# Kernel optimization log

Hardware: AMD Instinct MI355X
Metric: run time of the kernel (lower is better)

## Reference

```python
import jax, jax.numpy as jnp
import numpy as np

N = 100_000          # number of nodes
E = 3_200_000        # number of edges (avg degree 32)
IN_CH = 128
OUT_CH = 128


def setup_inputs() -> dict:
    key = jax.random.key(0)
    k1, k2, k3, k4 = jax.random.split(key, 4)
    x = jax.random.normal(k1, (N, IN_CH), dtype=jnp.float32)
    edge_index = jax.random.randint(k2, (2, E), 0, N, dtype=jnp.int32)
    # torch nn.Linear weights have shape [out_features, in_features]
    W_theta = jax.random.normal(k3, (OUT_CH, IN_CH), dtype=jnp.float32) / np.sqrt(IN_CH).astype(np.float32)
    W_phi = jax.random.normal(k4, (OUT_CH, OUT_CH), dtype=jnp.float32) / np.sqrt(OUT_CH).astype(np.float32)
    return {"x": x, "edge_index": edge_index, "W_theta": W_theta, "W_phi": W_phi}


def reference(x, edge_index, W_theta, W_phi):
    row, col = edge_index[0], edge_index[1]
    rel_pos = x[row] - x[col]                       # [E, in]
    rel_t = rel_pos @ W_theta.T                     # [E, out]
    aggr = jax.ops.segment_max(rel_t, row, num_segments=N)  # [N, out], -inf for empty segments
    # torch_scatter.scatter_max leaves empty segments at 0
    aggr = jnp.where(jnp.isneginf(aggr), jnp.zeros((), dtype=aggr.dtype), aggr)
    return aggr @ W_phi.T                           # [N, out]
```

## Files before the change

kernel.cpp:

```cpp
#include <hip/hip_runtime.h>
#include <stdint.h>

#define N_NODES 100000
#define N_EDGES 3200000
#define CH 128
#define NBUK 391
#define SPLIT_BLOCKS 391
#define CAP 8704

typedef __bf16 bf16x8 __attribute__((ext_vector_type(8)));
typedef float  floatx4 __attribute__((ext_vector_type(4)));

__device__ __forceinline__ unsigned short f2bf_bits(float f) {
    unsigned u = __float_as_uint(f);
    u += 0x7FFFu + ((u >> 16) & 1u);
    return (unsigned short)(u >> 16);
}

__device__ __forceinline__ unsigned short enc16(unsigned short b) {
    return b ^ ((b & 0x8000u) ? 0xFFFFu : 0x8000u);
}

__device__ __forceinline__ unsigned pkminu(unsigned a, unsigned b) {
    unsigned d;
    asm("v_pk_min_u16 %0, %1, %2" : "=v"(d) : "v"(a), "v"(b));
    return d;
}

__device__ __forceinline__ unsigned dec2(unsigned k) {
    unsigned lo = k & 0xFFFFu;
    unsigned hi = k >> 16;
    lo ^= (lo & 0x8000u) ? 0x8000u : 0xFFFFu;
    hi ^= (hi & 0x8000u) ? 0x8000u : 0xFFFFu;
    return lo | (hi << 16);
}

__device__ __forceinline__ bf16x8 pack8(floatx4 f0, floatx4 f1) {
    bf16x8 r;
    r[0] = (__bf16)f0[0]; r[1] = (__bf16)f0[1]; r[2] = (__bf16)f0[2]; r[3] = (__bf16)f0[3];
    r[4] = (__bf16)f1[0]; r[5] = (__bf16)f1[1]; r[6] = (__bf16)f1[2]; r[7] = (__bf16)f1[3];
    return r;
}

__global__ void k_setup(const float* __restrict__ Wt, const float* __restrict__ Wp,
                        unsigned short* __restrict__ wb, int* __restrict__ cursor) {
    int bid = blockIdx.x, t = threadIdx.x;
    if (bid < 128) {
        int i = bid * 256 + t;
        float v = (i < 16384) ? Wt[i] : Wp[i - 16384];
        wb[i] = f2bf_bits(v);
    } else {
        for (int i = t; i < NBUK; i += 256) cursor[i] = i * CAP;
    }
}

__global__ void k_split_gemmy(const int* __restrict__ row, const int* __restrict__ col,
                              int* __restrict__ cursor, int2* __restrict__ pairs,
                              const float* __restrict__ x,
                              const unsigned short* __restrict__ wb,
                              unsigned short* __restrict__ yt) {
    __shared__ int h[NBUK];
    __shared__ int basebuf[NBUK];
    int bid = blockIdx.x, t = threadIdx.x;
    if (bid < SPLIT_BLOCKS) {
        for (int i = t; i < NBUK; i += 256) h[i] = 0;
        __syncthreads();
        int e0 = bid * 8192;
#pragma unroll
        for (int j = 0; j < 8; j++) {
            int idx = e0 + j * 1024 + t * 4;
            if (idx < N_EDGES) {
                int4 r = *(const int4*)(row + idx);
                atomicAdd(&h[r.x >> 8], 1);
                atomicAdd(&h[r.y >> 8], 1);
                atomicAdd(&h[r.z >> 8], 1);
                atomicAdd(&h[r.w >> 8], 1);
            }
        }
        __syncthreads();
        for (int i = t; i < NBUK; i += 256) {
            int c = h[i];
            basebuf[i] = c ? atomicAdd(&cursor[i], c) : 0;
            h[i] = 0;
        }
        __syncthreads();
#pragma unroll
        for (int j = 0; j < 8; j++) {
            int idx = e0 + j * 1024 + t * 4;
            if (idx < N_EDGES) {
                int4 r = *(const int4*)(row + idx);
                int4 c = *(const int4*)(col + idx);
                int b, p;
                b = r.x >> 8; p = atomicAdd(&h[b], 1); pairs[basebuf[b] + p] = make_int2(r.x, c.x);
                b = r.y >> 8; p = atomicAdd(&h[b], 1); pairs[basebuf[b] + p] = make_int2(r.y, c.y);
                b = r.z >> 8; p = atomicAdd(&h[b], 1); pairs[basebuf[b] + p] = make_int2(r.z, c.z);
                b = r.w >> 8; p = atomicAdd(&h[b], 1); pairs[basebuf[b] + p] = make_int2(r.w, c.w);
            }
        }
    } else {
        int wave = ((bid - SPLIT_BLOCKS) * 256 + t) >> 6;
        int lane = t & 63;
        int row0 = wave * 16;
        if (row0 >= N_NODES) return;
        int m = lane & 15, quad = lane >> 4;

        bf16x8 a[4];
        const floatx4* xp = (const floatx4*)(x + (size_t)(row0 + m) * CH + quad * 8);
#pragma unroll
        for (int ks = 0; ks < 4; ks++) a[ks] = pack8(xp[ks * 8], xp[ks * 8 + 1]);

        for (int nt = 0; nt < 8; nt++) {
            const bf16x8* wp = (const bf16x8*)(wb + (size_t)(nt * 16 + m) * CH + quad * 8);
            floatx4 acc = {0.f, 0.f, 0.f, 0.f};
#pragma unroll
            for (int ks = 0; ks < 4; ks++)
                acc = __builtin_amdgcn_mfma_f32_16x16x32_bf16(a[ks], wp[ks * 4], acc, 0, 0, 0);
#pragma unroll
            for (int r = 0; r < 4; r++) {
                int orow = row0 + quad * 4 + r;
                yt[(size_t)orow * CH + nt * 16 + m] = enc16(f2bf_bits(acc[r]));
            }
        }
    }
}

__global__ void k_build(int2* __restrict__ pairs, const int* __restrict__ cursor,
                        int* __restrict__ deg, int* __restrict__ offs) {
    __shared__ int hist[256];
    __shared__ int sc[256];
    __shared__ int cur[256];
    __shared__ int lcsr[CAP];
    int b = blockIdx.x, t = threadIdx.x;
    int s0 = b * CAP;
    int cnt = cursor[b] - s0;
    if (cnt > CAP) cnt = CAP;
    hist[t] = 0;
    __syncthreads();
    for (int i = t; i < cnt; i += 256) {
        int2 p = pairs[s0 + i];
        atomicAdd(&hist[p.x & 255], 1);
    }
    __syncthreads();
    int d = hist[t];
    sc[t] = d;
    __syncthreads();
    for (int off = 1; off < 256; off <<= 1) {
        int v = (t >= off) ? sc[t - off] : 0;
        __syncthreads();
        sc[t] += v;
        __syncthreads();
    }
    int excl = sc[t] - d;
    int node = b * 256 + t;
    if (node < N_NODES) {
        deg[node] = d;
        offs[node] = 2 * s0 + excl;
    }
    cur[t] = excl;
    __syncthreads();
    for (int i = t; i < cnt; i += 256) {
        int2 p = pairs[s0 + i];
        int pos = atomicAdd(&cur[p.x & 255], 1);
        lcsr[pos] = p.y;
    }
    __syncthreads();
    int* csr = (int*)pairs;
    for (int i = t; i < cnt; i += 256) csr[2 * s0 + i] = lcsr[i];
}

#define PKA(v)                        \
    do {                              \
        m0 = pkminu(m0, (v).x);       \
        m1 = pkminu(m1, (v).y);       \
        m2 = pkminu(m2, (v).z);       \
        m3 = pkminu(m3, (v).w);       \
    } while (0)

__global__ void k_minaggr_out(const uint4* __restrict__ yt, const int* __restrict__ offs,
                              const int* __restrict__ deg, const int* __restrict__ csr,
                              const unsigned short* __restrict__ wb,
                              float* __restrict__ out) {
    __shared__ unsigned short atile[16 * 136];
    int t = threadIdx.x;
    int wave = t >> 6, lane = t & 63;
    int q = lane >> 4, s = lane & 15;
    int nl = wave * 4 + q;
    int n = blockIdx.x * 16 + nl;

    int i = offs[n];
    int len = deg[n];
    int end = i + len;

    unsigned m0 = ~0u, m1 = ~0u, m2 = ~0u, m3 = ~0u;

    for (; i + 8 <= end; i += 8) {
        int c0 = csr[i + 0];
        int c1 = csr[i + 1];
        int c2 = csr[i + 2];
        int c3 = csr[i + 3];
        int c4 = csr[i + 4];
        int c5 = csr[i + 5];
        int c6 = csr[i + 6];
        int c7 = csr[i + 7];
        uint4 v0 = yt[(size_t)c0 * 16 + s];
        uint4 v1 = yt[(size_t)c1 * 16 + s];
        uint4 v2 = yt[(size_t)c2 * 16 + s];
        uint4 v3 = yt[(size_t)c3 * 16 + s];
        uint4 v4 = yt[(size_t)c4 * 16 + s];
        uint4 v5 = yt[(size_t)c5 * 16 + s];
        uint4 v6 = yt[(size_t)c6 * 16 + s];
        uint4 v7 = yt[(size_t)c7 * 16 + s];
        PKA(v0); PKA(v1); PKA(v2); PKA(v3);
        PKA(v4); PKA(v5); PKA(v6); PKA(v7);
    }
    for (; i < end; i++) {
        int c = csr[i];
        uint4 v = yt[(size_t)c * 16 + s];
        PKA(v);
    }

    uint4 outv = {0u, 0u, 0u, 0u};
    if (len > 0) {
        unsigned d0 = dec2(m0), d1 = dec2(m1), d2 = dec2(m2), d3 = dec2(m3);
        uint4 se = yt[(size_t)n * 16 + s];
        unsigned s0 = dec2(se.x), s1 = dec2(se.y), s2 = dec2(se.z), s3 = dec2(se.w);
        outv.x = (unsigned)f2bf_bits(__uint_as_float(s0 << 16) - __uint_as_float(d0 << 16)) |
                 ((unsigned)f2bf_bits(__uint_as_float(s0 & 0xFFFF0000u) -
                                      __uint_as_float(d0 & 0xFFFF0000u)) << 16);
        outv.y = (unsigned)f2bf_bits(__uint_as_float(s1 << 16) - __uint_as_float(d1 << 16)) |
                 ((unsigned)f2bf_bits(__uint_as_float(s1 & 0xFFFF0000u) -
                                      __uint_as_float(d1 & 0xFFFF0000u)) << 16);
        outv.z = (unsigned)f2bf_bits(__uint_as_float(s2 << 16) - __uint_as_float(d2 << 16)) |
                 ((unsigned)f2bf_bits(__uint_as_float(s2 & 0xFFFF0000u) -
                                      __uint_as_float(d2 & 0xFFFF0000u)) << 16);
        outv.w = (unsigned)f2bf_bits(__uint_as_float(s3 << 16) - __uint_as_float(d3 << 16)) |
                 ((unsigned)f2bf_bits(__uint_as_float(s3 & 0xFFFF0000u) -
                                      __uint_as_float(d3 & 0xFFFF0000u)) << 16);
    }
    *(uint4*)&atile[nl * 136 + s * 8] = outv;
    __syncthreads();

    int m = lane & 15, quad = lane >> 4;
    bf16x8 a[4];
#pragma unroll
    for (int ks = 0; ks < 4; ks++)
        a[ks] = *(const bf16x8*)&atile[m * 136 + ks * 32 + quad * 8];

#pragma unroll
    for (int ntl = 0; ntl < 2; ntl++) {
        int nt = wave * 2 + ntl;
        const bf16x8* wp = (const bf16x8*)(wb + (size_t)(nt * 16 + m) * CH + quad * 8);
        floatx4 acc = {0.f, 0.f, 0.f, 0.f};
#pragma unroll
        for (int ks = 0; ks < 4; ks++)
            acc = __builtin_amdgcn_mfma_f32_16x16x32_bf16(a[ks], wp[ks * 4], acc, 0, 0, 0);
#pragma unroll
        for (int r = 0; r < 4; r++)
            out[(size_t)(blockIdx.x * 16 + quad * 4 + r) * CH + nt * 16 + m] = acc[r];
    }
}

extern "C" void kernel_launch(void* const* d_in, const int* in_sizes, int n_in,
                              void* d_out, int out_size, void* d_ws, size_t ws_size,
                              hipStream_t stream) {
    const float* x   = (const float*)d_in[0];
    const int* edge  = (const int*)d_in[1];
    const float* Wt  = (const float*)d_in[2];
    const float* Wp  = (const float*)d_in[3];
    const int* row = edge;
    const int* col = edge + N_EDGES;
    float* out = (float*)d_out;

    char* ws = (char*)d_ws;
    int* deg    = (int*)ws;  ws += 400128;
    int* offs   = (int*)ws;  ws += 400128;
    int* cursor = (int*)ws;  ws += 2048;
    unsigned short* yt = (unsigned short*)ws; ws += 25600000;
    unsigned short* wb = (unsigned short*)ws; ws += 65536;
    int2* pairs = (int2*)ws; ws += (size_t)NBUK * CAP * 8;

    k_setup<<<129, 256, 0, stream>>>(Wt, Wp, wb, cursor);
    k_split_gemmy<<<SPLIT_BLOCKS + 1563, 256, 0, stream>>>(row, col, cursor, pairs,
                                                           x, wb, yt);
    k_build<<<NBUK, 256, 0, stream>>>(pairs, cursor, deg, offs);
    k_minaggr_out<<<N_NODES / 16, 256, 0, stream>>>((const uint4*)yt, offs, deg,
                                                    (const int*)pairs, wb + 16384, out);
}
```

Before: 308.6 us.

## Pack edge pairs into 32-bit words and co-schedule the GEMM with the CSR build

Edge pairs are packed into one 32-bit word (local row index in the high bits, column in the low 17 bits), which halves the scatter and readback traffic. The split stage now runs as its own kernel with more, smaller blocks and registers holding the row loads. The bucket CSR build is fused with the x·Wθ GEMM in one 1024-thread kernel so the two stages overlap. This adds a bounds check on bucket capacity, but the larger blocks also raise LDS and register pressure, which could limit occupancy.

```diff
diff --git a/kernel.cpp b/kernel.cpp
--- a/kernel.cpp
+++ b/kernel.cpp
@@ -5,8 +5,8 @@
 #define N_EDGES 3200000
 #define CH 128
 #define NBUK 391
-#define SPLIT_BLOCKS 391
 #define CAP 8704
+#define SPLIT_BLOCKS 1563
 
 typedef __bf16 bf16x8 __attribute__((ext_vector_type(8)));
 typedef float  floatx4 __attribute__((ext_vector_type(4)));
@@ -54,53 +54,107 @@
     }
 }
 
-__global__ void k_split_gemmy(const int* __restrict__ row, const int* __restrict__ col,
-                              int* __restrict__ cursor, int2* __restrict__ pairs,
+__global__ void k_split(const int* __restrict__ row, const int* __restrict__ col,
+                        int* __restrict__ cursor, unsigned* __restrict__ pairs) {
+    __shared__ int h[NBUK];
+    __shared__ int basebuf[NBUK];
+    int bid = blockIdx.x, t = threadIdx.x;
+    for (int i = t; i < NBUK; i += 256) h[i] = 0;
+    __syncthreads();
+    int e0 = bid * 2048;
+    int4 r[2];
+    bool v[2];
+#pragma unroll
+    for (int j = 0; j < 2; j++) {
+        int idx = e0 + j * 1024 + t * 4;
+        v[j] = idx < N_EDGES;
+        if (v[j]) {
+            r[j] = *(const int4*)(row + idx);
+            atomicAdd(&h[r[j].x >> 8], 1);
+            atomicAdd(&h[r[j].y >> 8], 1);
+            atomicAdd(&h[r[j].z >> 8], 1);
+            atomicAdd(&h[r[j].w >> 8], 1);
+        }
+    }
+    __syncthreads();
+    for (int i = t; i < NBUK; i += 256) {
+        int c = h[i];
+        basebuf[i] = c ? atomicAdd(&cursor[i], c) : 0;
+        h[i] = 0;
+    }
+    __syncthreads();
+#pragma unroll
+    for (int j = 0; j < 2; j++) {
+        if (v[j]) {
+            int idx = e0 + j * 1024 + t * 4;
+            int4 c = *(const int4*)(col + idx);
+            int b, p;
+            b = r[j].x >> 8; p = basebuf[b] + atomicAdd(&h[b], 1);
+            if (p < (b + 1) * CAP) pairs[p] = ((unsigned)(r[j].x & 255) << 17) | (unsigned)c.x;
+            b = r[j].y >> 8; p = basebuf[b] + atomicAdd(&h[b], 1);
+            if (p < (b + 1) * CAP) pairs[p] = ((unsigned)(r[j].y & 255) << 17) | (unsigned)c.y;
+            b = r[j].z >> 8; p = basebuf[b] + atomicAdd(&h[b], 1);
+            if (p < (b + 1) * CAP) pairs[p] = ((unsigned)(r[j].z & 255) << 17) | (unsigned)c.z;
+            b = r[j].w >> 8; p = basebuf[b] + atomicAdd(&h[b], 1);
+            if (p < (b + 1) * CAP) pairs[p] = ((unsigned)(r[j].w & 255) << 17) | (unsigned)c.w;
+        }
+    }
+}
+
+__global__ void k_build_gemmy(unsigned* __restrict__ pairs, const int* __restrict__ cursor,
+                              int* __restrict__ deg, int* __restrict__ offs,
                               const float* __restrict__ x,
                               const unsigned short* __restrict__ wb,
                               unsigned short* __restrict__ yt) {
-    __shared__ int h[NBUK];
-    __shared__ int basebuf[NBUK];
     int bid = blockIdx.x, t = threadIdx.x;
-    if (bid < SPLIT_BLOCKS) {
-        for (int i = t; i < NBUK; i += 256) h[i] = 0;
-        __syncthreads();
-        int e0 = bid * 8192;
-#pragma unroll
-        for (int j = 0; j < 8; j++) {
-            int idx = e0 + j * 1024 + t * 4;
-            if (idx < N_EDGES) {
-                int4 r = *(const int4*)(row + idx);
-                atomicAdd(&h[r.x >> 8], 1);
-                atomicAdd(&h[r.y >> 8], 1);
-                atomicAdd(&h[r.z >> 8], 1);
-                atomicAdd(&h[r.w >> 8], 1);
+    if (bid < NBUK) {
+        __shared__ int hist[256];
+        __shared__ int sc[256];
+        __shared__ int cur[256];
+        __shared__ int lcsr[CAP];
+        int b = bid;
+        int s0 = b * CAP;
+        int cnt = cursor[b] - s0;
+        if (cnt > CAP) cnt = CAP;
+        if (t < 256) hist[t] = 0;
+        __syncthreads();
+        for (int i = t; i < cnt; i += 1024) {
+            unsigned p = pairs[s0 + i];
+            atomicAdd(&hist[p >> 17], 1);
+        }
+        __syncthreads();
+        int d = 0;
+        if (t < 256) { d = hist[t]; sc[t] = d; }
+        __syncthreads();
+        for (int off = 1; off < 256; off <<= 1) {
+            int vv = 0;
+            if (t < 256 && t >= off) vv = sc[t - off];
+            __syncthreads();
+            if (t < 256) sc[t] += vv;
+            __syncthreads();
+        }
+        if (t < 256) {
+            int excl = sc[t] - d;
+            int node = b * 256 + t;
+            if (node < N_NODES) {
+                deg[node] = d;
+                offs[node] = s0 + excl;
             }
-        }
-        __syncthreads();
-        for (int i = t; i < NBUK; i += 256) {
-            int c = h[i];
-            basebuf[i] = c ? atomicAdd(&cursor[i], c) : 0;
-            h[i] = 0;
-        }
-        __syncthreads();
-#pragma unroll
-        for (int j = 0; j < 8; j++) {
-            int idx = e0 + j * 1024 + t * 4;
-            if (idx < N_EDGES) {
-                int4 r = *(const int4*)(row + idx);
-                int4 c = *(const int4*)(col + idx);
-                int b, p;
-                b = r.x >> 8; p = atomicAdd(&h[b], 1); pairs[basebuf[b] + p] = make_int2(r.x, c.x);
-                b = r.y >> 8; p = atomicAdd(&h[b], 1); pairs[basebuf[b] + p] = make_int2(r.y, c.y);
-                b = r.z >> 8; p = atomicAdd(&h[b], 1); pairs[basebuf[b] + p] = make_int2(r.z, c.z);
-                b = r.w >> 8; p = atomicAdd(&h[b], 1); pairs[basebuf[b] + p] = make_int2(r.w, c.w);
-            }
-        }
+            cur[t] = excl;
+        }
+        __syncthreads();
+        for (int i = t; i < cnt; i += 1024) {
+            unsigned p = pairs[s0 + i];
+            int pos = atomicAdd(&cur[p >> 17], 1);
+            lcsr[pos] = (int)(p & 0x1FFFFu);
+        }
+        __syncthreads();
+        int* csr = (int*)pairs;
+        for (int i = t; i < cnt; i += 1024) csr[s0 + i] = lcsr[i];
     } else {
-        int wave = ((bid - SPLIT_BLOCKS) * 256 + t) >> 6;
+        int w = (bid - NBUK) * 16 + (t >> 6);
         int lane = t & 63;
-        int row0 = wave * 16;
+        int row0 = w * 16;
         if (row0 >= N_NODES) return;
         int m = lane & 15, quad = lane >> 4;
 
@@ -122,50 +176,6 @@
             }
         }
     }
-}
-
-__global__ void k_build(int2* __restrict__ pairs, const int* __restrict__ cursor,
-                        int* __restrict__ deg, int* __restrict__ offs) {
-    __shared__ int hist[256];
-    __shared__ int sc[256];
-    __shared__ int cur[256];
-    __shared__ int lcsr[CAP];
-    int b = blockIdx.x, t = threadIdx.x;
-    int s0 = b * CAP;
-    int cnt = cursor[b] - s0;
-    if (cnt > CAP) cnt = CAP;
-    hist[t] = 0;
-    __syncthreads();
-    for (int i = t; i < cnt; i += 256) {
-        int2 p = pairs[s0 + i];
-        atomicAdd(&hist[p.x & 255], 1);
-    }
-    __syncthreads();
-    int d = hist[t];
-    sc[t] = d;
-    __syncthreads();
-    for (int off = 1; off < 256; off <<= 1) {
-        int v = (t >= off) ? sc[t - off] : 0;
-        __syncthreads();
-        sc[t] += v;
-        __syncthreads();
-    }
-    int excl = sc[t] - d;
-    int node = b * 256 + t;
-    if (node < N_NODES) {
-        deg[node] = d;
-        offs[node] = 2 * s0 + excl;
-    }
-    cur[t] = excl;
-    __syncthreads();
-    for (int i = t; i < cnt; i += 256) {
-        int2 p = pairs[s0 + i];
-        int pos = atomicAdd(&cur[p.x & 255], 1);
-        lcsr[pos] = p.y;
-    }
-    __syncthreads();
-    int* csr = (int*)pairs;
-    for (int i = t; i < cnt; i += 256) csr[2 * s0 + i] = lcsr[i];
 }
 
 #define PKA(v)                        \
@@ -277,12 +287,11 @@
     int* cursor = (int*)ws;  ws += 2048;
     unsigned short* yt = (unsigned short*)ws; ws += 25600000;
     unsigned short* wb = (unsigned short*)ws; ws += 65536;
-    int2* pairs = (int2*)ws; ws += (size_t)NBUK * CAP * 8;
+    unsigned* pairs = (unsigned*)ws; ws += (size_t)NBUK * CAP * 4;
 
     k_setup<<<129, 256, 0, stream>>>(Wt, Wp, wb, cursor);
-    k_split_gemmy<<<SPLIT_BLOCKS + 1563, 256, 0, stream>>>(row, col, cursor, pairs,
-                                                           x, wb, yt);
-    k_build<<<NBUK, 256, 0, stream>>>(pairs, cursor, deg, offs);
+    k_split<<<SPLIT_BLOCKS, 256, 0, stream>>>(row, col, cursor, pairs);
+    k_build_gemmy<<<NBUK + 391, 1024, 0, stream>>>(pairs, cursor, deg, offs, x, wb, yt);
     k_minaggr_out<<<N_NODES / 16, 256, 0, stream>>>((const uint4*)yt, offs, deg,
                                                     (const int*)pairs, wb + 16384, out);
 }
```

After: 337.5 us. 1.09x slower.
